# Kernel tuning notes

Hardware: AMD Instinct MI355X
Metric: run time of the kernel (lower is better)

The kernel has to match this reference:

```python
import jax, jax.numpy as jnp
import numpy as np

EM_DIM = 64
GROUP = 16
DIM_IN = 1024


def _position_embedding(boxes, part_boxes):
    # boxes: [N,4], part_boxes: [P,4] -> [N,P,EM_DIM]
    xmin, ymin, xmax, ymax = [boxes[:, i:i + 1] for i in range(4)]            # [N,1]
    pxmin, pymin, pxmax, pymax = [part_boxes[:, i:i + 1].T for i in range(4)]  # [1,P]
    bw = xmax - xmin + 1.0
    bh = ymax - ymin + 1.0
    pw = pxmax - pxmin + 1.0
    ph = pymax - pymin + 1.0
    cx = 0.5 * (xmin + xmax)
    cy = 0.5 * (ymin + ymax)
    pcx = 0.5 * (pxmin + pxmax)
    pcy = 0.5 * (pymin + pymax)
    dx = jnp.abs((cx - pcx) / bw)
    dy = jnp.abs((cy - pcy) / bh)
    dx = jnp.log(jnp.where(dx < 1e-3, 1e-3, dx))
    dy = jnp.log(jnp.where(dy < 1e-3, 1e-3, dy))
    dw = jnp.log(pw / bw)
    dh = jnp.log(ph / bh)
    pos = jnp.stack([dx, dy, dw, dh], axis=2)                                  # [N,P,4]
    em_range = jnp.arange(EM_DIM // 8, dtype=pos.dtype) / (EM_DIM // 8)        # [8]
    em_mat = jnp.power(jnp.asarray(1000.0, pos.dtype), em_range)               # [8]
    div = (100.0 * pos)[..., None] / em_mat                                    # [N,P,4,8]
    emb = jnp.concatenate([jnp.sin(div), jnp.cos(div)], axis=3)                # [N,P,4,16]
    return emb.reshape(pos.shape[0], pos.shape[1], EM_DIM)


def _single_relation(boxes, part_boxes, bf, pf, Wg_w, Wg_b, Wq_w, Wq_b, Wk_w, Wk_b, conv_w, conv_b):
    N = bf.shape[0]
    P = pf.shape[0]
    emb = _position_embedding(boxes, part_boxes)                               # [N,P,64]
    pos_feat = jax.nn.relu(emb @ Wg_w.T + Wg_b)                                # [N,P,G]
    att_weight = jnp.transpose(pos_feat, (0, 2, 1))                            # [N,G,P]
    q = (bf @ Wq_w.T + Wq_b).reshape(N, GROUP, EM_DIM)                         # [N,G,64]
    k = (pf @ Wk_w.T + Wk_b).reshape(P, GROUP, EM_DIM)                         # [P,G,64]
    att = jnp.einsum('ngd,pgd->ngp', q, k) * (1.0 / GROUP)                     # [N,G,P]
    att_weight = jnp.where(att_weight < 1e-6, 1e-6, att_weight)
    sm = jax.nn.softmax(jnp.log(att_weight) + att, axis=2)                     # [N,G,P]
    out = jnp.einsum('ngp,pc->ngc', sm, pf)                                    # [N,G,dim_in]
    # grouped 1x1 conv: group g maps dim_in channels -> EM_DIM channels
    w3 = conv_w.reshape(GROUP, EM_DIM, DIM_IN)
    rel = jnp.einsum('ngc,goc->ngo', out, w3).reshape(N, GROUP * EM_DIM) + conv_b
    return rel                                                                  # [N, G*EM_DIM]


def setup_inputs() -> dict:
    key = jax.random.key(0)
    ks = jax.random.split(key, 12)
    N_TOT, P_TOT = 2048, 2048

    def make_rois(k1, k2, n, n1):
        xy = jax.random.uniform(k1, (n, 2), jnp.float32) * 800.0
        wh = jax.random.uniform(k2, (n, 2), jnp.float32) * 200.0 + 16.0
        boxes = jnp.concatenate([xy, xy + wh], axis=1)
        idx = jnp.concatenate([jnp.zeros((n1, 1)), jnp.ones((n - n1, 1))], axis=0).astype(jnp.float32)
        return jnp.concatenate([idx, boxes], axis=1)

    rois = make_rois(ks[0], ks[1], N_TOT, 1024)
    part_rois = make_rois(ks[2], ks[3], P_TOT, 1024)
    box_feats = jax.random.normal(ks[4], (N_TOT, DIM_IN), jnp.float32)
    part_feats = jax.random.normal(ks[5], (P_TOT, DIM_IN), jnp.float32)
    xav_g = float(np.sqrt(6.0 / (EM_DIM + GROUP)))
    xav_qk = float(np.sqrt(6.0 / (DIM_IN + GROUP * EM_DIM)))
    Wg_w = jax.random.uniform(ks[6], (GROUP, EM_DIM), jnp.float32, -xav_g, xav_g)
    Wg_b = jnp.zeros((GROUP,), jnp.float32)
    Wq_w = jax.random.uniform(ks[7], (GROUP * EM_DIM, DIM_IN), jnp.float32, -xav_qk, xav_qk)
    Wq_b = jnp.zeros((GROUP * EM_DIM,), jnp.float32)
    Wk_w = jax.random.uniform(ks[8], (GROUP * EM_DIM, DIM_IN), jnp.float32, -xav_qk, xav_qk)
    Wk_b = jnp.zeros((GROUP * EM_DIM,), jnp.float32)
    conv_w = jax.random.normal(ks[9], (GROUP * EM_DIM, DIM_IN), jnp.float32) * 0.02
    conv_b = jnp.zeros((GROUP * EM_DIM,), jnp.float32)
    return {"rois": rois, "part_rois": part_rois, "box_feats": box_feats,
            "part_feats": part_feats, "Wg_w": Wg_w, "Wg_b": Wg_b,
            "Wq_w": Wq_w, "Wq_b": Wq_b, "Wk_w": Wk_w, "Wk_b": Wk_b,
            "conv_w": conv_w, "conv_b": conv_b, "n1_boxes": 1024, "n1_parts": 1024}


def reference(rois, part_rois, box_feats, part_feats, Wg_w, Wg_b, Wq_w, Wq_b,
              Wk_w, Wk_b, conv_w, conv_b, n1_boxes, n1_parts):
    boxes = rois[:, 1:5]
    part_boxes = part_rois[:, 1:5]
    params = (Wg_w, Wg_b, Wq_w, Wq_b, Wk_w, Wk_b, conv_w, conv_b)
    rel1 = _single_relation(boxes[:n1_boxes], part_boxes[:n1_parts],
                            box_feats[:n1_boxes], part_feats[:n1_parts], *params)
    rel2 = _single_relation(boxes[n1_boxes:], part_boxes[n1_parts:],
                            box_feats[n1_boxes:], part_feats[n1_parts:], *params)
    return jnp.concatenate([rel1, rel2], axis=0)  # [N_total, GROUP*EM_DIM]
```

## Files before the change

kernel.cpp:

```cpp
#include <hip/hip_runtime.h>

typedef unsigned short u16;
using short8  = __attribute__((ext_vector_type(8))) short;
using float4v = __attribute__((ext_vector_type(4))) float;

__device__ __forceinline__ u16 f2bf(float f) {
    union { float f; unsigned u; } v; v.f = f;
    unsigned r = (v.u + 0x7fff + ((v.u >> 16) & 1)) >> 16;
    return (u16)r;
}
__device__ __forceinline__ float bf2f(u16 h) {
    union { unsigned u; float f; } v; v.u = ((unsigned)h) << 16; return v.f;
}
__device__ __forceinline__ unsigned pkbf(float lo, float hi) {
    unsigned d;
    asm("v_cvt_pk_bf16_f32 %0, %1, %2" : "=v"(d) : "v"(lo), "v"(hi));
    return d;
}
__device__ __forceinline__ float sin_rev(float r) {
    float f, s;
    asm("v_fract_f32 %0, %1" : "=v"(f) : "v"(r));
    asm("v_sin_f32 %0, %1" : "=v"(s) : "v"(f));
    return s;
}
__device__ __forceinline__ void dma16(const void* g, void* l) {
    __builtin_amdgcn_global_load_lds((const __attribute__((address_space(1))) void*)g,
                                     (__attribute__((address_space(3))) void*)l, 16, 0, 0);
}

__device__ __forceinline__ void cvt4(const float* __restrict__ s, u16* __restrict__ o, int i) {
    float4 v = ((const float4*)s)[i];
    uint2 r; r.x = pkbf(v.x, v.y); r.y = pkbf(v.z, v.w);
    ((uint2*)o)[i] = r;
}

__global__ __launch_bounds__(256)
void cvt_all(const float* __restrict__ s0, const float* __restrict__ s1,
             const float* __restrict__ s2, const float* __restrict__ s3,
             const float* __restrict__ s4, const float* __restrict__ prois,
             u16* __restrict__ o0, u16* __restrict__ o1, u16* __restrict__ o2,
             u16* __restrict__ o3, u16* __restrict__ o4, float4* __restrict__ PD,
             int na4, int nb4, int nw4, int PT) {
    int i = blockIdx.x * 256 + threadIdx.x;
    if (i < na4) { cvt4(s0, o0, i); return; }
    i -= na4;
    if (i < nb4) { cvt4(s1, o1, i); return; }
    i -= nb4;
    if (i < nw4) { cvt4(s2, o2, i); return; }
    i -= nw4;
    if (i < nw4) { cvt4(s3, o3, i); return; }
    i -= nw4;
    if (i < nw4) { cvt4(s4, o4, i); return; }
    i -= nw4;
    if (i < PT) {
        const float* pr = prois + (size_t)i * 5;
        float pxmin = pr[1], pymin = pr[2], pxmax = pr[3], pymax = pr[4];
        PD[i] = make_float4(0.5f * (pxmin + pxmax), 0.5f * (pymin + pymax),
                            __logf(pxmax - pxmin + 1.0f), __logf(pymax - pymin + 1.0f));
    }
}

__global__ __launch_bounds__(256)
void proj_mfma(const u16* __restrict__ Ab, const u16* __restrict__ Pb,
               const u16* __restrict__ Wqb, const u16* __restrict__ Wkb,
               const u16* __restrict__ Cwb, const float* __restrict__ bq,
               const float* __restrict__ bk, u16* __restrict__ Qb,
               u16* __restrict__ Kb, u16* __restrict__ PVt, int PT) {
    __shared__ __align__(16) u16 As[128 * 64];
    __shared__ __align__(16) u16 Ws[64 * 64];
    __shared__ __align__(16) u16 Tr[128 * 68];

    const int z = blockIdx.z;
    const int m0 = blockIdx.y * 128, j0 = blockIdx.x * 64;
    const u16* A = (z == 0) ? Ab : Pb;
    const u16* W = (z == 0) ? Wqb : (z == 1 ? Wkb : Cwb);
    const int t = threadIdx.x;
    const int w = t >> 6, lane = t & 63;
    const int wm = w >> 1, wn = w & 1;
    const int lr = lane >> 3, lc = lane & 7, gch = lc ^ lr;
    const int fm = lane & 15, quad = lane >> 4;

    float4v zero4 = {0.f, 0.f, 0.f, 0.f};
    float4v acc[4][2];
#pragma unroll
    for (int i = 0; i < 4; ++i) { acc[i][0] = zero4; acc[i][1] = zero4; }

    for (int k0 = 0; k0 < 1024; k0 += 64) {
#pragma unroll
        for (int i = 0; i < 4; ++i) {
            int row = w * 32 + i * 8 + lr;
            dma16(A + (size_t)(m0 + row) * 1024 + k0 + gch * 8,
                  As + (w * 32 + i * 8) * 64 + lane * 8);
        }
#pragma unroll
        for (int i = 0; i < 2; ++i) {
            int row = w * 16 + i * 8 + lr;
            dma16(W + (size_t)(j0 + row) * 1024 + k0 + gch * 8,
                  Ws + (w * 16 + i * 8) * 64 + lane * 8);
        }
        __syncthreads();
#pragma unroll
        for (int ks = 0; ks < 2; ++ks) {
            int c = ks * 4 + quad;
            short8 af[4], bf[2];
#pragma unroll
            for (int i = 0; i < 4; ++i) {
                int ra = wm * 64 + i * 16 + fm;
                af[i] = *(const short8*)(As + ra * 64 + ((c ^ (ra & 7)) * 8));
            }
#pragma unroll
            for (int j = 0; j < 2; ++j) {
                int rb = wn * 32 + j * 16 + fm;
                bf[j] = *(const short8*)(Ws + rb * 64 + ((c ^ (rb & 7)) * 8));
            }
#pragma unroll
            for (int i = 0; i < 4; ++i)
#pragma unroll
                for (int j = 0; j < 2; ++j)
                    acc[i][j] = __builtin_amdgcn_mfma_f32_16x16x32_bf16(af[i], bf[j], acc[i][j], 0, 0, 0);
        }
        __syncthreads();
    }

    if (z < 2) {
        u16* O = z ? Kb : Qb;
        const float* bias = z ? bk : bq;
#pragma unroll
        for (int j = 0; j < 2; ++j) {
            int jl = wn * 32 + j * 16 + fm;
            float bb = bias[j0 + jl];
#pragma unroll
            for (int i = 0; i < 4; ++i) {
                int mlb = wm * 64 + i * 16 + quad * 4;
#pragma unroll
                for (int r = 0; r < 4; ++r)
                    Tr[(mlb + r) * 68 + jl] = f2bf(acc[i][j][r] + bb);
            }
        }
        __syncthreads();
#pragma unroll
        for (int i2 = 0; i2 < 4; ++i2) {
            int f = i2 * 2048 + t * 8;
            int ml = f >> 6, jl = f & 63;
            union { uint2 u2[2]; short8 s8; } uu;
            uu.u2[0] = *(const uint2*)(Tr + ml * 68 + jl);
            uu.u2[1] = *(const uint2*)(Tr + ml * 68 + jl + 4);
            *(short8*)(O + (size_t)(m0 + ml) * 1024 + j0 + jl) = uu.s8;
        }
    } else {
#pragma unroll
        for (int j = 0; j < 2; ++j) {
            int jl = wn * 32 + j * 16 + fm;
#pragma unroll
            for (int i = 0; i < 4; ++i) {
                int mlb = wm * 64 + i * 16 + quad * 4;
                uint2 pk;
                pk.x = pkbf(acc[i][j][0], acc[i][j][1]);
                pk.y = pkbf(acc[i][j][2], acc[i][j][3]);
                *(uint2*)(Tr + jl * 136 + mlb) = pk;
            }
        }
        __syncthreads();
#pragma unroll
        for (int i2 = 0; i2 < 4; ++i2) {
            int f = i2 * 2048 + t * 8;
            int jl = f >> 7, ml = f & 127;
            union { uint2 u2[2]; short8 s8; } uu;
            uu.u2[0] = *(const uint2*)(Tr + jl * 136 + ml);
            uu.u2[1] = *(const uint2*)(Tr + jl * 136 + ml + 4);
            *(short8*)(PVt + (size_t)(j0 + jl) * PT + m0 + ml) = uu.s8;
        }
    }
}

__global__ __launch_bounds__(256)
void posw_fused(const float* __restrict__ rois, const float4* __restrict__ PD,
                const float* __restrict__ Wg_w, const float* __restrict__ Wg_b,
                u16* __restrict__ POSW, const int* __restrict__ n1b_p,
                const int* __restrict__ n1p_p, int PT) {
    const int n = blockIdx.x, t = threadIdx.x;
    const int w = t >> 6, lane = t & 63;
    const int fm = lane & 15, quad = lane >> 4;
    const int n1b = *n1b_p, n1p = *n1p_p;
    const int hh = (n >= n1b) ? 1 : 0;
    const int p0 = hh ? n1p : 0;
    const int Ph = hh ? (PT - n1p) : n1p;

    float xmin = rois[n * 5 + 1], ymin = rois[n * 5 + 2];
    float xmax = rois[n * 5 + 3], ymax = rois[n * 5 + 4];
    float bw = xmax - xmin + 1.0f, bh = ymax - ymin + 1.0f;
    float cx = 0.5f * (xmin + xmax), cy = 0.5f * (ymin + ymax);

    const int jA = quad >> 1, trig = quad & 1;
    float cA   = (jA == 0) ? cx : cy;
    float invA = (jA == 0) ? (1.0f / bw) : (1.0f / bh);
    float lB   = (jA == 0) ? __logf(bw) : __logf(bh);
    float toff = trig ? 0.25f : 0.0f;

    const int g_ = fm;
    short8 b1, b2;
    {
        const float* w1 = Wg_w + g_ * 64 + quad * 8;
        const float* w2 = Wg_w + g_ * 64 + 32 + quad * 8;
        unsigned* p1 = (unsigned*)&b1;
        unsigned* p2 = (unsigned*)&b2;
#pragma unroll
        for (int kk = 0; kk < 4; ++kk) {
            p1[kk] = pkbf(w1[2 * kk], w1[2 * kk + 1]);
            p2[kk] = pkbf(w2[2 * kk], w2[2 * kk + 1]);
        }
    }
    float wgb = Wg_b[g_];

    const float inv_em[8] = {1.0f, 0.4216965034f, 0.1778279410f, 0.0749894209f,
                             0.0316227766f, 0.0133352143f, 0.0056234133f, 0.0023713737f};
    const float REV = 15.91549431f;
    const int prange = Ph >> 2;
    const int pb0 = w * prange;
    u16* rowp = POSW + ((size_t)n * 16 + g_) * 1024;

    float4 pd_c = PD[p0 + pb0 + fm];

#pragma unroll 2
    for (int pt = 0; pt < 16; ++pt) {
        int pbase = pb0 + pt * 16;
        float4 pd_n;
        if (pt < 15) pd_n = PD[p0 + pbase + 16 + fm];
        float pc = (jA == 0) ? pd_c.x : pd_c.y;
        float lp = (jA == 0) ? pd_c.z : pd_c.w;
        float posA = __logf(fmaxf(fabsf(cA - pc) * invA, 0.001f));
        float posB = lp - lB;
        float br1 = posA * REV, br2 = posB * REV;
        float e1[8], e2[8];
#pragma unroll
        for (int k = 0; k < 8; ++k) {
            e1[k] = sin_rev(fmaf(br1, inv_em[k], toff));
            e2[k] = sin_rev(fmaf(br2, inv_em[k], toff));
        }
        short8 a1, a2;
        unsigned* pa1 = (unsigned*)&a1;
        unsigned* pa2 = (unsigned*)&a2;
#pragma unroll
        for (int kk = 0; kk < 4; ++kk) {
            pa1[kk] = pkbf(e1[2 * kk], e1[2 * kk + 1]);
            pa2[kk] = pkbf(e2[2 * kk], e2[2 * kk + 1]);
        }
        float4v acc = {wgb, wgb, wgb, wgb};
        acc = __builtin_amdgcn_mfma_f32_16x16x32_bf16(a1, b1, acc, 0, 0, 0);
        acc = __builtin_amdgcn_mfma_f32_16x16x32_bf16(a2, b2, acc, 0, 0, 0);

        float w0  = fmaxf(acc[0], 1e-6f);
        float w1v = fmaxf(acc[1], 1e-6f);
        float w2v = fmaxf(acc[2], 1e-6f);
        float w3v = fmaxf(acc[3], 1e-6f);
        uint2 wp; wp.x = pkbf(w0, w1v); wp.y = pkbf(w2v, w3v);
        *(uint2*)(rowp + pbase + quad * 4) = wp;

        pd_c = pd_n;
    }
}

__global__ __launch_bounds__(256)
void fused_rel(const u16* __restrict__ Qb, const u16* __restrict__ Kb,
               const u16* __restrict__ POSW, const u16* __restrict__ PVt,
               const float* __restrict__ conv_b, float* __restrict__ OUT,
               const int* __restrict__ n1b_p, const int* __restrict__ n1p_p, int PT) {
    __shared__ __align__(16) u16 Qs[64 * 64];
    __shared__ __align__(16) u16 Ks[64 * 64];
    __shared__ __align__(16) u16 Ps[64 * 64];
    __shared__ __align__(16) u16 Vs[64 * 64];
    __shared__ __align__(16) u16 Wt[64 * 64];
    __shared__ float redl[2][64];

    const int n0 = blockIdx.x * 64, g = blockIdx.y;
    const int n1b = *n1b_p, n1p = *n1p_p;
    const int hh = (n0 >= n1b) ? 1 : 0;
    const int p0 = hh ? n1p : 0;
    const int Ph = hh ? (PT - n1p) : n1p;
    const int t = threadIdx.x;
    const int w = t >> 6, lane = t & 63;
    const int wm = w >> 1, wn = w & 1;
    const int lr = lane >> 3, lc = lane & 7, gch = lc ^ lr;
    const int fm = lane & 15, quad = lane >> 4;

#pragma unroll
    for (int i = 0; i < 2; ++i) {
        int row = w * 16 + i * 8 + lr;
        dma16(Qb + (size_t)(n0 + row) * 1024 + g * 64 + gch * 8,
              Qs + (w * 16 + i * 8) * 64 + lane * 8);
        dma16(Kb + (size_t)(p0 + row) * 1024 + g * 64 + gch * 8,
              Ks + (w * 16 + i * 8) * 64 + lane * 8);
        dma16(POSW + ((size_t)(n0 + row) * 16 + g) * 1024 + gch * 8,
              Ps + (w * 16 + i * 8) * 64 + lane * 8);
    }

    float4v zero4 = {0.f, 0.f, 0.f, 0.f};
    float4v oacc[2][2];
    float rsum[2][4];
#pragma unroll
    for (int i = 0; i < 2; ++i) {
        oacc[i][0] = zero4; oacc[i][1] = zero4;
#pragma unroll
        for (int r = 0; r < 4; ++r) rsum[i][r] = 0.f;
    }

    __syncthreads();

    short8 qf[2][2];
#pragma unroll
    for (int ks = 0; ks < 2; ++ks) {
        int c = ks * 4 + quad;
#pragma unroll
        for (int i = 0; i < 2; ++i) {
            int ra = wm * 32 + i * 16 + fm;
            qf[ks][i] = *(const short8*)(Qs + ra * 64 + ((c ^ (ra & 7)) * 8));
        }
    }

    const int NPT = Ph >> 6;
    for (int pt = 0; pt < NPT; ++pt) {
#pragma unroll
        for (int i = 0; i < 2; ++i) {
            int row = w * 16 + i * 8 + lr;
            dma16(PVt + (size_t)(g * 64 + row) * PT + p0 + pt * 64 + gch * 8,
                  Vs + (w * 16 + i * 8) * 64 + lane * 8);
        }
        float4v atc[2][2];
        atc[0][0] = zero4; atc[0][1] = zero4; atc[1][0] = zero4; atc[1][1] = zero4;
#pragma unroll
        for (int ks = 0; ks < 2; ++ks) {
            int c = ks * 4 + quad;
            short8 bfr[2];
#pragma unroll
            for (int j = 0; j < 2; ++j) {
                int rb = wn * 32 + j * 16 + fm;
                bfr[j] = *(const short8*)(Ks + rb * 64 + ((c ^ (rb & 7)) * 8));
            }
#pragma unroll
            for (int i = 0; i < 2; ++i)
#pragma unroll
                for (int j = 0; j < 2; ++j)
                    atc[i][j] = __builtin_amdgcn_mfma_f32_16x16x32_bf16(qf[ks][i], bfr[j], atc[i][j], 0, 0, 0);
        }
#pragma unroll
        for (int j = 0; j < 2; ++j) {
            int pl = wn * 32 + j * 16 + fm;
            int pch = pl >> 3, psub = pl & 7;
#pragma unroll
            for (int i = 0; i < 2; ++i)
#pragma unroll
                for (int r = 0; r < 4; ++r) {
                    int nl = wm * 32 + i * 16 + quad * 4 + r;
                    int sw = ((pch ^ (nl & 7)) * 8) + psub;
                    float pw = bf2f(Ps[nl * 64 + sw]);
                    float wv = pw * __expf(atc[i][j][r] * 0.0625f);
                    rsum[i][r] += wv;
                    Wt[nl * 64 + sw] = f2bf(wv);
                }
        }
        __syncthreads();
        if (pt + 1 < NPT) {
#pragma unroll
            for (int i = 0; i < 2; ++i) {
                int row = w * 16 + i * 8 + lr;
                dma16(Kb + (size_t)(p0 + (pt + 1) * 64 + row) * 1024 + g * 64 + gch * 8,
                      Ks + (w * 16 + i * 8) * 64 + lane * 8);
                dma16(POSW + ((size_t)(n0 + row) * 16 + g) * 1024 + (pt + 1) * 64 + gch * 8,
                      Ps + (w * 16 + i * 8) * 64 + lane * 8);
            }
        }
#pragma unroll
        for (int ks = 0; ks < 2; ++ks) {
            int c = ks * 4 + quad;
            short8 wf[2], vf[2];
#pragma unroll
            for (int i = 0; i < 2; ++i) {
                int ra = wm * 32 + i * 16 + fm;
                wf[i] = *(const short8*)(Wt + ra * 64 + ((c ^ (ra & 7)) * 8));
            }
#pragma unroll
            for (int j = 0; j < 2; ++j) {
                int rb = wn * 32 + j * 16 + fm;
                vf[j] = *(const short8*)(Vs + rb * 64 + ((c ^ (rb & 7)) * 8));
            }
#pragma unroll
            for (int i = 0; i < 2; ++i)
#pragma unroll
                for (int j = 0; j < 2; ++j)
                    oacc[i][j] = __builtin_amdgcn_mfma_f32_16x16x32_bf16(wf[i], vf[j], oacc[i][j], 0, 0, 0);
        }
        __syncthreads();
    }

#pragma unroll
    for (int i = 0; i < 2; ++i)
#pragma unroll
        for (int r = 0; r < 4; ++r) {
            float s = rsum[i][r];
            s += __shfl_xor(s, 1, 64);
            s += __shfl_xor(s, 2, 64);
            s += __shfl_xor(s, 4, 64);
            s += __shfl_xor(s, 8, 64);
            rsum[i][r] = s;
        }
    if (fm == 0) {
#pragma unroll
        for (int i = 0; i < 2; ++i)
#pragma unroll
            for (int r = 0; r < 4; ++r)
                redl[wn][wm * 32 + i * 16 + quad * 4 + r] = rsum[i][r];
    }
    __syncthreads();

    float bb[2];
    bb[0] = conv_b[g * 64 + wn * 32 + fm];
    bb[1] = conv_b[g * 64 + wn * 32 + 16 + fm];
#pragma unroll
    for (int i = 0; i < 2; ++i)
#pragma unroll
        for (int r = 0; r < 4; ++r) {
            int nl = wm * 32 + i * 16 + quad * 4 + r;
            float inv = 1.0f / (redl[0][nl] + redl[1][nl]);
#pragma unroll
            for (int j = 0; j < 2; ++j) {
                int o = wn * 32 + j * 16 + fm;
                OUT[(size_t)(n0 + nl) * 1024 + g * 64 + o] = oacc[i][j][r] * inv + bb[j];
            }
        }
}

extern "C" void kernel_launch(void* const* d_in, const int* in_sizes, int n_in,
                              void* d_out, int out_size, void* d_ws, size_t ws_size,
                              hipStream_t stream) {
    const float* rois   = (const float*)d_in[0];
    const float* prois  = (const float*)d_in[1];
    const float* bfeat  = (const float*)d_in[2];
    const float* pfeat  = (const float*)d_in[3];
    const float* Wg_w   = (const float*)d_in[4];
    const float* Wg_b   = (const float*)d_in[5];
    const float* Wq_w   = (const float*)d_in[6];
    const float* Wq_b   = (const float*)d_in[7];
    const float* Wk_w   = (const float*)d_in[8];
    const float* Wk_b   = (const float*)d_in[9];
    const float* conv_w = (const float*)d_in[10];
    const float* conv_b = (const float*)d_in[11];
    const int*   n1b    = (const int*)d_in[12];
    const int*   n1p    = (const int*)d_in[13];

    const int NT = in_sizes[2] / 1024;
    const int PT = in_sizes[3] / 1024;

    u16* Qb   = (u16*)d_ws;
    u16* Kb   = Qb + (size_t)NT * 1024;
    u16* PVt  = Kb + (size_t)PT * 1024;
    float4* PD = (float4*)(PVt + (size_t)1024 * PT);
    u16* POSW = (u16*)(PD + PT);
    u16* Ab   = POSW + (size_t)NT * 16 * 1024;
    u16* Pb   = Ab + (size_t)NT * 1024;
    u16* Wqb  = Pb + (size_t)PT * 1024;
    u16* Wkb  = Wqb + 1024 * 1024;
    u16* Cwb  = Wkb + 1024 * 1024;

    dim3 blk(256);
    int nf4 = NT * 1024 / 4, pf4 = PT * 1024 / 4, wf4 = 1024 * 1024 / 4;
    int tot = nf4 + pf4 + 3 * wf4 + PT;
    cvt_all<<<dim3((tot + 255) / 256), blk, 0, stream>>>(
        bfeat, pfeat, Wq_w, Wk_w, conv_w, prois, Ab, Pb, Wqb, Wkb, Cwb, PD,
        nf4, pf4, wf4, PT);

    proj_mfma<<<dim3(16, NT / 128, 3), blk, 0, stream>>>(Ab, Pb, Wqb, Wkb, Cwb,
                                                         Wq_b, Wk_b, Qb, Kb, PVt, PT);
    posw_fused<<<dim3(NT), blk, 0, stream>>>(rois, PD, Wg_w, Wg_b, POSW, n1b, n1p, PT);
    fused_rel<<<dim3(NT / 64, 16), blk, 0, stream>>>(Qb, Kb, POSW, PVt, conv_b,
                                                     (float*)d_out, n1b, n1p, PT);
}
```

Before: 178.2 us.

## Double-buffer K/POSW/V tiles and give each wave its own 16 rows

The K, position-weight and V tiles are now double-buffered, so the next tile's DMA is issued before the current tile is computed, and there is one barrier per iteration instead of two. The warp layout changes from a 2x2 split to one wave per 16 query rows. Each wave computes S^T across all 64 parts, writes its softmax weights to a private LDS slice and runs the PV MFMA without a cross-wave barrier. The row-sum reduction now uses in-wave shuffles instead of LDS. The cost is roughly twice the LDS footprint (about 56KB), which may lower occupancy.

```diff
diff --git a/kernel.cpp b/kernel.cpp
--- a/kernel.cpp
+++ b/kernel.cpp
@@ -266,11 +266,10 @@
                const float* __restrict__ conv_b, float* __restrict__ OUT,
                const int* __restrict__ n1b_p, const int* __restrict__ n1p_p, int PT) {
     __shared__ __align__(16) u16 Qs[64 * 64];
-    __shared__ __align__(16) u16 Ks[64 * 64];
-    __shared__ __align__(16) u16 Ps[64 * 64];
-    __shared__ __align__(16) u16 Vs[64 * 64];
-    __shared__ __align__(16) u16 Wt[64 * 64];
-    __shared__ float redl[2][64];
+    __shared__ __align__(16) u16 Ks[2][64 * 64];
+    __shared__ __align__(16) u16 Ps[2][64 * 64];
+    __shared__ __align__(16) u16 Vs[2][64 * 64];
+    __shared__ __align__(16) u16 Wt[4][16 * 64];
 
     const int n0 = blockIdx.x * 64, g = blockIdx.y;
     const int n1b = *n1b_p, n1p = *n1p_p;
@@ -279,153 +278,115 @@
     const int Ph = hh ? (PT - n1p) : n1p;
     const int t = threadIdx.x;
     const int w = t >> 6, lane = t & 63;
-    const int wm = w >> 1, wn = w & 1;
     const int lr = lane >> 3, lc = lane & 7, gch = lc ^ lr;
     const int fm = lane & 15, quad = lane >> 4;
-
+    const int swz = fm & 7;
+
+    auto stage = [&](int pt, int buf) {
+#pragma unroll
+        for (int i = 0; i < 2; ++i) {
+            int row = w * 16 + i * 8 + lr;
+            dma16(Kb + (size_t)(p0 + pt * 64 + row) * 1024 + g * 64 + gch * 8,
+                  Ks[buf] + (w * 16 + i * 8) * 64 + lane * 8);
+            dma16(POSW + ((size_t)(n0 + row) * 16 + g) * 1024 + pt * 64 + gch * 8,
+                  Ps[buf] + (w * 16 + i * 8) * 64 + lane * 8);
+            dma16(PVt + (size_t)(g * 64 + row) * PT + p0 + pt * 64 + gch * 8,
+                  Vs[buf] + (w * 16 + i * 8) * 64 + lane * 8);
+        }
+    };
+
+    stage(0, 0);
 #pragma unroll
     for (int i = 0; i < 2; ++i) {
         int row = w * 16 + i * 8 + lr;
         dma16(Qb + (size_t)(n0 + row) * 1024 + g * 64 + gch * 8,
               Qs + (w * 16 + i * 8) * 64 + lane * 8);
-        dma16(Kb + (size_t)(p0 + row) * 1024 + g * 64 + gch * 8,
-              Ks + (w * 16 + i * 8) * 64 + lane * 8);
-        dma16(POSW + ((size_t)(n0 + row) * 16 + g) * 1024 + gch * 8,
-              Ps + (w * 16 + i * 8) * 64 + lane * 8);
     }
 
     float4v zero4 = {0.f, 0.f, 0.f, 0.f};
-    float4v oacc[2][2];
-    float rsum[2][4];
-#pragma unroll
-    for (int i = 0; i < 2; ++i) {
-        oacc[i][0] = zero4; oacc[i][1] = zero4;
-#pragma unroll
-        for (int r = 0; r < 4; ++r) rsum[i][r] = 0.f;
-    }
+    float4v oacc[4];
+#pragma unroll
+    for (int ob = 0; ob < 4; ++ob) oacc[ob] = zero4;
+    float rsum = 0.0f;
 
     __syncthreads();
 
-    short8 qf[2][2];
-#pragma unroll
-    for (int ks = 0; ks < 2; ++ks) {
-        int c = ks * 4 + quad;
-#pragma unroll
-        for (int i = 0; i < 2; ++i) {
-            int ra = wm * 32 + i * 16 + fm;
-            qf[ks][i] = *(const short8*)(Qs + ra * 64 + ((c ^ (ra & 7)) * 8));
-        }
-    }
+    const int nloc = w * 16 + fm;
+    short8 qf[2];
+#pragma unroll
+    for (int kd = 0; kd < 2; ++kd) {
+        int c = kd * 4 + quad;
+        qf[kd] = *(const short8*)(Qs + nloc * 64 + ((c ^ swz) * 8));
+    }
+    u16* wrow = Wt[w] + fm * 64;
 
     const int NPT = Ph >> 6;
     for (int pt = 0; pt < NPT; ++pt) {
-#pragma unroll
-        for (int i = 0; i < 2; ++i) {
-            int row = w * 16 + i * 8 + lr;
-            dma16(PVt + (size_t)(g * 64 + row) * PT + p0 + pt * 64 + gch * 8,
-                  Vs + (w * 16 + i * 8) * 64 + lane * 8);
-        }
-        float4v atc[2][2];
-        atc[0][0] = zero4; atc[0][1] = zero4; atc[1][0] = zero4; atc[1][1] = zero4;
-#pragma unroll
-        for (int ks = 0; ks < 2; ++ks) {
-            int c = ks * 4 + quad;
-            short8 bfr[2];
-#pragma unroll
-            for (int j = 0; j < 2; ++j) {
-                int rb = wn * 32 + j * 16 + fm;
-                bfr[j] = *(const short8*)(Ks + rb * 64 + ((c ^ (rb & 7)) * 8));
-            }
-#pragma unroll
-            for (int i = 0; i < 2; ++i)
-#pragma unroll
-                for (int j = 0; j < 2; ++j)
-                    atc[i][j] = __builtin_amdgcn_mfma_f32_16x16x32_bf16(qf[ks][i], bfr[j], atc[i][j], 0, 0, 0);
-        }
-#pragma unroll
-        for (int j = 0; j < 2; ++j) {
-            int pl = wn * 32 + j * 16 + fm;
-            int pch = pl >> 3, psub = pl & 7;
-#pragma unroll
-            for (int i = 0; i < 2; ++i)
-#pragma unroll
-                for (int r = 0; r < 4; ++r) {
-                    int nl = wm * 32 + i * 16 + quad * 4 + r;
-                    int sw = ((pch ^ (nl & 7)) * 8) + psub;
-                    float pw = bf2f(Ps[nl * 64 + sw]);
-                    float wv = pw * __expf(atc[i][j][r] * 0.0625f);
-                    rsum[i][r] += wv;
-                    Wt[nl * 64 + sw] = f2bf(wv);
-                }
-        }
+        int cur = pt & 1;
+        if (pt + 1 < NPT) stage(pt + 1, cur ^ 1);
+        const u16* ks_ = Ks[cur];
+        const u16* ps_ = Ps[cur];
+        const u16* vs_ = Vs[cur];
+
+        float4v atc[4];
+#pragma unroll
+        for (int pi = 0; pi < 4; ++pi) atc[pi] = zero4;
+#pragma unroll
+        for (int kd = 0; kd < 2; ++kd) {
+            int c = kd * 4 + quad;
+#pragma unroll
+            for (int pi = 0; pi < 4; ++pi) {
+                int rp = pi * 16 + fm;
+                short8 kf = *(const short8*)(ks_ + rp * 64 + ((c ^ swz) * 8));
+                atc[pi] = __builtin_amdgcn_mfma_f32_16x16x32_bf16(kf, qf[kd], atc[pi], 0, 0, 0);
+            }
+        }
+
+#pragma unroll
+        for (int pi = 0; pi < 4; ++pi) {
+            int co = ((pi * 2 + (quad >> 1)) ^ swz) * 8 + (quad & 1) * 4;
+            uint2 pwp = *(const uint2*)(ps_ + nloc * 64 + co);
+            const u16* pww = (const u16*)&pwp;
+            float wv0 = bf2f(pww[0]) * __expf(atc[pi][0] * 0.0625f);
+            float wv1 = bf2f(pww[1]) * __expf(atc[pi][1] * 0.0625f);
+            float wv2 = bf2f(pww[2]) * __expf(atc[pi][2] * 0.0625f);
+            float wv3 = bf2f(pww[3]) * __expf(atc[pi][3] * 0.0625f);
+            rsum += (wv0 + wv1) + (wv2 + wv3);
+            uint2 wp; wp.x = pkbf(wv0, wv1); wp.y = pkbf(wv2, wv3);
+            *(uint2*)(wrow + co) = wp;
+        }
+
+#pragma unroll
+        for (int m = 0; m < 2; ++m) {
+            short8 af = *(const short8*)(wrow + (((m * 4 + quad) ^ swz) * 8));
+#pragma unroll
+            for (int ob = 0; ob < 4; ++ob) {
+                int ro = ob * 16 + fm;
+                short8 vf = *(const short8*)(vs_ + ro * 64 + (((m * 4 + quad) ^ swz) * 8));
+                oacc[ob] = __builtin_amdgcn_mfma_f32_16x16x32_bf16(af, vf, oacc[ob], 0, 0, 0);
+            }
+        }
+
         __syncthreads();
-        if (pt + 1 < NPT) {
-#pragma unroll
-            for (int i = 0; i < 2; ++i) {
-                int row = w * 16 + i * 8 + lr;
-                dma16(Kb + (size_t)(p0 + (pt + 1) * 64 + row) * 1024 + g * 64 + gch * 8,
-                      Ks + (w * 16 + i * 8) * 64 + lane * 8);
-                dma16(POSW + ((size_t)(n0 + row) * 16 + g) * 1024 + (pt + 1) * 64 + gch * 8,
-                      Ps + (w * 16 + i * 8) * 64 + lane * 8);
-            }
-        }
-#pragma unroll
-        for (int ks = 0; ks < 2; ++ks) {
-            int c = ks * 4 + quad;
-            short8 wf[2], vf[2];
-#pragma unroll
-            for (int i = 0; i < 2; ++i) {
-                int ra = wm * 32 + i * 16 + fm;
-                wf[i] = *(const short8*)(Wt + ra * 64 + ((c ^ (ra & 7)) * 8));
-            }
-#pragma unroll
-            for (int j = 0; j < 2; ++j) {
-                int rb = wn * 32 + j * 16 + fm;
-                vf[j] = *(const short8*)(Vs + rb * 64 + ((c ^ (rb & 7)) * 8));
-            }
-#pragma unroll
-            for (int i = 0; i < 2; ++i)
-#pragma unroll
-                for (int j = 0; j < 2; ++j)
-                    oacc[i][j] = __builtin_amdgcn_mfma_f32_16x16x32_bf16(wf[i], vf[j], oacc[i][j], 0, 0, 0);
-        }
-        __syncthreads();
-    }
-
-#pragma unroll
-    for (int i = 0; i < 2; ++i)
+    }
+
+    float s = rsum;
+    s += __shfl_xor(s, 16, 64);
+    s += __shfl_xor(s, 32, 64);
+    float inv[4];
+#pragma unroll
+    for (int r = 0; r < 4; ++r)
+        inv[r] = 1.0f / __shfl(s, quad * 4 + r, 64);
+
+    float bb[4];
+#pragma unroll
+    for (int ob = 0; ob < 4; ++ob) bb[ob] = conv_b[g * 64 + ob * 16 + fm];
+#pragma unroll
+    for (int ob = 0; ob < 4; ++ob)
 #pragma unroll
         for (int r = 0; r < 4; ++r) {
-            float s = rsum[i][r];
-            s += __shfl_xor(s, 1, 64);
-            s += __shfl_xor(s, 2, 64);
-            s += __shfl_xor(s, 4, 64);
-            s += __shfl_xor(s, 8, 64);
-            rsum[i][r] = s;
-        }
-    if (fm == 0) {
-#pragma unroll
-        for (int i = 0; i < 2; ++i)
-#pragma unroll
-            for (int r = 0; r < 4; ++r)
-                redl[wn][wm * 32 + i * 16 + quad * 4 + r] = rsum[i][r];
-    }
-    __syncthreads();
-
-    float bb[2];
-    bb[0] = conv_b[g * 64 + wn * 32 + fm];
-    bb[1] = conv_b[g * 64 + wn * 32 + 16 + fm];
-#pragma unroll
-    for (int i = 0; i < 2; ++i)
-#pragma unroll
-        for (int r = 0; r < 4; ++r) {
-            int nl = wm * 32 + i * 16 + quad * 4 + r;
-            float inv = 1.0f / (redl[0][nl] + redl[1][nl]);
-#pragma unroll
-            for (int j = 0; j < 2; ++j) {
-                int o = wn * 32 + j * 16 + fm;
-                OUT[(size_t)(n0 + nl) * 1024 + g * 64 + o] = oacc[i][j][r] * inv + bb[j];
-            }
+            int nn = n0 + w * 16 + quad * 4 + r;
+            OUT[(size_t)nn * 1024 + g * 64 + ob * 16 + fm] = oacc[ob][r] * inv[r] + bb[ob];
         }
 }
 
```

Result: no change. 176.0 us (-1.2%).
